# Kernel tuning notes

Measured on AMD Instinct MI355X. Metric: run time of the kernel, lower is better.

Reference implementation:

```python
import jax, jax.numpy as jnp
import numpy as np

N = 8192
F_IN = 1024
F_OUT = 256
ALPHA = 0.2          # LeakyReLU negative slope
ADJ_DENSITY = 0.004  # pre-symmetrization edge probability -> avg degree ~65
NEG_INF = -9.0e15    # matches -9000000000000000.0 in the torch code


def setup_inputs() -> dict:
    key = jax.random.key(0)
    k_h, k_W, k_a, k_adj = jax.random.split(key, 4)
    h = jax.random.normal(k_h, (N, F_IN), dtype=jnp.float32)
    # xavier_uniform with gain=1.414
    lim_W = 1.414 * np.sqrt(6.0 / (F_IN + F_OUT))
    W = jax.random.uniform(k_W, (F_IN, F_OUT), dtype=jnp.float32, minval=-lim_W, maxval=lim_W)
    lim_a = 1.414 * np.sqrt(6.0 / (2 * F_OUT + 1))
    a = jax.random.uniform(k_a, (2 * F_OUT, 1), dtype=jnp.float32, minval=-lim_a, maxval=lim_a)
    # sparse symmetric 0/1 adjacency (float, like the torch code's dense adj)
    u = jax.random.uniform(k_adj, (N, N))
    m = u < ADJ_DENSITY
    adj = (m | m.T).astype(jnp.float32)
    return {"h": h, "adj": adj, "W": W, "a": a}


def reference(h, adj, W, a):
    # --- GAT attention ---
    Wh = h @ W                                   # [N, F_OUT]
    Wh1 = Wh @ a[:F_OUT]                          # [N, 1]
    Wh2 = Wh @ a[F_OUT:]                          # [N, 1]
    e = jax.nn.leaky_relu(Wh1 + Wh2.T, negative_slope=ALPHA)   # [N, N]
    attention = jax.nn.softmax(jnp.where(adj > 0, e, NEG_INF), axis=1)

    # --- per-row variable-k pruning of attention + attention@attention.T ---
    n = adj.shape[0]
    diag = jnp.eye(n, dtype=bool)
    adj_nodiag = jnp.where(diag, 0.0, adj)
    s2 = jnp.count_nonzero(adj_nodiag, axis=1)    # [N] int, variable k per row

    attention2step = attention @ attention.T      # [N, N] dense GEMM
    comb = attention + attention2step
    comb = jnp.where(diag, 0.0, comb)

    # threshold = s2[i]-th largest value of row i (np.partition(row, -k)[-k])
    sorted_desc = -jnp.sort(-comb, axis=1)        # [N, N] descending per row
    idx = jnp.maximum(s2 - 1, 0)[:, None]         # clamp for s2==0 rows
    thr = jnp.take_along_axis(sorted_desc, idx, axis=1)   # [N, 1]
    # keep values >= threshold (torch code zeros values strictly < partition);
    # rows with s2 == 0 are zeroed entirely
    pruned = jnp.where((s2[:, None] > 0) & (comb >= thr), comb, 0.0)
    adj_resize = (pruned > 0).astype(jnp.float32)

    # --- output (eval mode: dropout is identity); concat=True -> ELU ---
    h_prime = attention @ Wh                      # [N, F_OUT]
    return jax.nn.elu(h_prime), adj_resize
```

## Files before the change

### kernel.cpp

```cpp
#include <hip/hip_runtime.h>
#include <cstdint>
#include <cstddef>

#define NN 8192
#define KFIN 1024
#define KFOUT 256
#define MAXD 192
#define LRALPHA 0.2f

typedef float f32x4 __attribute__((ext_vector_type(4)));

__global__ void __launch_bounds__(256) k_build_csr(
    const float* __restrict__ adj, int* __restrict__ nbr,
    int* __restrict__ deg, int* __restrict__ s2v) {
  const int wave = threadIdx.x >> 6;
  const int lane = threadIdx.x & 63;
  const int row = blockIdx.x * 4 + wave;
  const float* arow = adj + (size_t)row * NN;
  int* outp = nbr + (size_t)row * MAXD;
  int count = 0;
  int dflag = 0;
  const unsigned long long below = (1ull << lane) - 1ull;
  for (int c0 = 0; c0 < NN; c0 += 256) {
    const int c = c0 + lane * 4;
    const f32x4 v = __builtin_nontemporal_load(
        reinterpret_cast<const f32x4*>(arow + c));
    const unsigned long long m0 = __ballot(v[0] > 0.0f);
    const unsigned long long m1 = __ballot(v[1] > 0.0f);
    const unsigned long long m2 = __ballot(v[2] > 0.0f);
    const unsigned long long m3 = __ballot(v[3] > 0.0f);
    int pos = count + (int)(__popcll(m0 & below) + __popcll(m1 & below) +
                            __popcll(m2 & below) + __popcll(m3 & below));
    if (v[0] > 0.0f) { if (pos < MAXD) outp[pos] = c + 0; ++pos; if (c + 0 == row) dflag = 1; }
    if (v[1] > 0.0f) { if (pos < MAXD) outp[pos] = c + 1; ++pos; if (c + 1 == row) dflag = 1; }
    if (v[2] > 0.0f) { if (pos < MAXD) outp[pos] = c + 2; ++pos; if (c + 2 == row) dflag = 1; }
    if (v[3] > 0.0f) { if (pos < MAXD) outp[pos] = c + 3; ++pos; if (c + 3 == row) dflag = 1; }
    count += (int)(__popcll(m0) + __popcll(m1) + __popcll(m2) + __popcll(m3));
  }
  const int anyd = __any(dflag) ? 1 : 0;
  if (lane == 0) {
    deg[row] = count < MAXD ? count : MAXD;
    s2v[row] = count - anyd;
  }
}

__global__ void __launch_bounds__(256) k_gemm(
    const float* __restrict__ A, const float* __restrict__ B,
    float* __restrict__ C) {
  __shared__ float As[16][65];
  __shared__ float Bs[16][65];
  const int tid = threadIdx.x;
  const int brow = blockIdx.y * 64;
  const int bcol = blockIdx.x * 64;
  const int tx = tid & 15;
  const int ty = tid >> 4;
  float acc[4][4];
#pragma unroll
  for (int i = 0; i < 4; ++i)
#pragma unroll
    for (int j = 0; j < 4; ++j) acc[i][j] = 0.0f;
  const int ar = tid >> 2;
  const int ac = (tid & 3) << 2;
  const int br = tid >> 4;
  const int bc = (tid & 15) << 2;
  for (int k0 = 0; k0 < KFIN; k0 += 16) {
    const float4 av =
        *reinterpret_cast<const float4*>(A + (size_t)(brow + ar) * KFIN + k0 + ac);
    const float4 bv =
        *reinterpret_cast<const float4*>(B + (size_t)(k0 + br) * KFOUT + bcol + bc);
    As[ac + 0][ar] = av.x;
    As[ac + 1][ar] = av.y;
    As[ac + 2][ar] = av.z;
    As[ac + 3][ar] = av.w;
    Bs[br][bc + 0] = bv.x;
    Bs[br][bc + 1] = bv.y;
    Bs[br][bc + 2] = bv.z;
    Bs[br][bc + 3] = bv.w;
    __syncthreads();
#pragma unroll
    for (int kk = 0; kk < 16; ++kk) {
      const float a0 = As[kk][ty * 4 + 0];
      const float a1 = As[kk][ty * 4 + 1];
      const float a2 = As[kk][ty * 4 + 2];
      const float a3 = As[kk][ty * 4 + 3];
      const float b0 = Bs[kk][tx * 4 + 0];
      const float b1 = Bs[kk][tx * 4 + 1];
      const float b2 = Bs[kk][tx * 4 + 2];
      const float b3 = Bs[kk][tx * 4 + 3];
      acc[0][0] += a0 * b0; acc[0][1] += a0 * b1; acc[0][2] += a0 * b2; acc[0][3] += a0 * b3;
      acc[1][0] += a1 * b0; acc[1][1] += a1 * b1; acc[1][2] += a1 * b2; acc[1][3] += a1 * b3;
      acc[2][0] += a2 * b0; acc[2][1] += a2 * b1; acc[2][2] += a2 * b2; acc[2][3] += a2 * b3;
      acc[3][0] += a3 * b0; acc[3][1] += a3 * b1; acc[3][2] += a3 * b2; acc[3][3] += a3 * b3;
    }
    __syncthreads();
  }
#pragma unroll
  for (int i = 0; i < 4; ++i) {
#pragma unroll
    for (int j = 0; j < 4; ++j) {
      C[(size_t)(brow + ty * 4 + i) * KFOUT + bcol + tx * 4 + j] = acc[i][j];
    }
  }
}

__global__ void __launch_bounds__(256) k_rowdots(
    const float* __restrict__ Wh, const float* __restrict__ a,
    float* __restrict__ Wh1, float* __restrict__ Wh2) {
  __shared__ float sA[256];
  __shared__ float sB[256];
  const int row = blockIdx.x;
  const int t = threadIdx.x;
  const float w = Wh[(size_t)row * KFOUT + t];
  sA[t] = w * a[t];
  sB[t] = w * a[KFOUT + t];
  __syncthreads();
  for (int s = 128; s > 0; s >>= 1) {
    if (t < s) {
      sA[t] += sA[t + s];
      sB[t] += sB[t + s];
    }
    __syncthreads();
  }
  if (t == 0) {
    Wh1[row] = sA[0];
    Wh2[row] = sB[0];
  }
}

__global__ void __launch_bounds__(256) k_stats(
    const int* __restrict__ nbr, const int* __restrict__ deg,
    const float* __restrict__ Wh1, const float* __restrict__ Wh2,
    float* __restrict__ mrow, float* __restrict__ Zrow) {
  const int wave = threadIdx.x >> 6;
  const int lane = threadIdx.x & 63;
  const int row = blockIdx.x * 4 + wave;
  const int d = deg[row];
  const int* cols = nbr + (size_t)row * MAXD;
  const float w1 = Wh1[row];
  float mx = -1e30f;
  for (int t = lane; t < d; t += 64) {
    float e = w1 + Wh2[cols[t]];
    e = e > 0.0f ? e : LRALPHA * e;
    mx = fmaxf(mx, e);
  }
  for (int o = 32; o > 0; o >>= 1) mx = fmaxf(mx, __shfl_xor(mx, o));
  float sum = 0.0f;
  for (int t = lane; t < d; t += 64) {
    float e = w1 + Wh2[cols[t]];
    e = e > 0.0f ? e : LRALPHA * e;
    sum += expf(e - mx);
  }
  for (int o = 32; o > 0; o >>= 1) sum += __shfl_xor(sum, o);
  if (lane == 0) {
    mrow[row] = mx;
    Zrow[row] = (d > 0) ? sum : 1.0f;
  }
}

__global__ void __launch_bounds__(256) k_att(
    const int* __restrict__ nbr, const int* __restrict__ deg,
    const float* __restrict__ Wh1, const float* __restrict__ Wh2,
    const float* __restrict__ mrow, const float* __restrict__ Zrow,
    float* __restrict__ att, int2* __restrict__ edgesT,
    short* __restrict__ qb8) {
  const int wave = threadIdx.x >> 6;
  const int lane = threadIdx.x & 63;
  const int row = blockIdx.x * 4 + wave;
  const int d = deg[row];
  const int* cols = nbr + (size_t)row * MAXD;
  const float w1r = Wh1[row];
  const float w2r = Wh2[row];
  const float mr = mrow[row];
  const float invZr = 1.0f / Zrow[row];
  int b[7] = {0, 0, 0, 0, 0, 0, 0};
  for (int t0 = 0; t0 < d; t0 += 64) {
    const int t = t0 + lane;
    const bool act = t < d;
    const int j = act ? cols[t] : 0x7fffffff;
#pragma unroll
    for (int m = 1; m <= 7; ++m)
      b[m - 1] += (int)__popcll(__ballot(act && j < m * 1024));
    if (act) {
      float e = w1r + Wh2[j];
      e = e > 0.0f ? e : LRALPHA * e;
      att[(size_t)row * MAXD + t] = expf(e - mr) * invZr;
      float e2 = Wh1[j] + w2r;
      e2 = e2 > 0.0f ? e2 : LRALPHA * e2;
      const float v = expf(e2 - mrow[j]) / Zrow[j];
      edgesT[(size_t)row * MAXD + t] = make_int2(j, __float_as_int(v));
    }
  }
  if (lane == 0) {
    short* q = qb8 + (size_t)row * 8;
    q[0] = (short)b[0]; q[1] = (short)b[1]; q[2] = (short)b[2]; q[3] = (short)b[3];
    q[4] = (short)b[4]; q[5] = (short)b[5]; q[6] = (short)b[6]; q[7] = (short)d;
  }
}

__global__ void __launch_bounds__(512) k_twostep(
    const int* __restrict__ nbr, const int* __restrict__ deg,
    const int* __restrict__ s2v, const float* __restrict__ att,
    const int2* __restrict__ edgesT, const short* __restrict__ qb8,
    float* __restrict__ out1) {
  __shared__ float comb[NN];
  __shared__ float wvals[MAXD];
  __shared__ int kcols[MAXD];
  __shared__ int kbase[MAXD];
  __shared__ unsigned short packw[8][MAXD];
  __shared__ unsigned int hist[256];
  __shared__ unsigned int shPrefix;
  __shared__ int shRemaining;
  const int tid = threadIdx.x;
  const int wave = tid >> 6;
  const int lane = tid & 63;
  const int row = blockIdx.x;
  const f32x4 z4 = {0.0f, 0.0f, 0.0f, 0.0f};
  for (int j = tid * 4; j < NN; j += 2048)
    *reinterpret_cast<f32x4*>(&comb[j]) = z4;
  const int d = deg[row];
  const int* cols = nbr + (size_t)row * MAXD;
  const float* arow = att + (size_t)row * MAXD;
  for (int t = tid; t < d; t += 512) {
    const int c = cols[t];
    kcols[t] = c;
    kbase[t] = c * MAXD;
    wvals[t] = arow[t];
    short q[8];
    *reinterpret_cast<int4*>(q) = *reinterpret_cast<const int4*>(&qb8[(size_t)c * 8]);
    int prev = 0;
#pragma unroll
    for (int w = 0; w < 8; ++w) {
      const int qe = (int)q[w];
      packw[w][t] = (unsigned short)(prev | (qe << 8));
      prev = qe;
    }
  }
  __syncthreads();
  {
    const int grp = lane >> 4;
    const int sub = lane & 15;
    const int nsteps = (d + 3) >> 2;
    int2 eA = make_int2(0, 0), eB = make_int2(0, 0);
    float wA = 0.0f, wB = 0.0f;
    bool pA_ = false, pB_ = false;
#define PA_ISSUE(E_, W_, P_, S_)                                       \
    {                                                                   \
      const int t_ = (S_) * 4 + grp;                                    \
      const bool v_ = t_ < d;                                           \
      const unsigned pk_ = v_ ? (unsigned)packw[wave][t_] : 0u;         \
      const int qs_ = (int)(pk_ & 255u);                                \
      const int qe_ = (int)(pk_ >> 8);                                  \
      P_ = v_ && (qs_ + sub) < qe_;                                     \
      W_ = v_ ? wvals[t_] : 0.0f;                                       \
      E_ = make_int2(0, 0);                                             \
      if (P_) E_ = edgesT[(size_t)kbase[t_] + qs_ + sub];               \
    }
    if (nsteps > 0) PA_ISSUE(eA, wA, pA_, 0);
    if (nsteps > 1) PA_ISSUE(eB, wB, pB_, 1);
    for (int s = 0; s < nsteps; ++s) {
      const int2 e = eA; const float w = wA; const bool p = pA_;
      eA = eB; wA = wB; pA_ = pB_;
      if (s + 2 < nsteps) PA_ISSUE(eB, wB, pB_, s + 2);
      if (p) atomicAdd(&comb[e.x], w * __int_as_float(e.y));
    }
#undef PA_ISSUE
  }
  for (int t0 = 0; t0 < d; t0 += 64) {
    const int t = t0 + lane;
    bool big = false;
    if (t < d) {
      const unsigned pk = (unsigned)packw[wave][t];
      big = ((int)(pk >> 8) - (int)(pk & 255u)) > 16;
    }
    unsigned long long m = __ballot(big);
    while (m) {
      const int tt = t0 + (int)__ffsll((long long)m) - 1;
      m &= m - 1;
      const unsigned pk = (unsigned)packw[wave][tt];
      const int qs = (int)(pk & 255u);
      const int qe = (int)(pk >> 8);
      const float w = wvals[tt];
      const int base = kbase[tt];
      for (int off = qs + 16 + lane; off < qe; off += 64) {
        const int2 e = edgesT[(size_t)base + off];
        atomicAdd(&comb[e.x], w * __int_as_float(e.y));
      }
    }
  }
  {
    const short* qr = qb8 + (size_t)row * 8;
    const int qlo = wave ? (int)qr[wave - 1] : 0;
    const int qhi = (int)qr[wave];
    for (int t = qlo + lane; t < qhi; t += 64) comb[kcols[t]] += wvals[t];
  }
  __syncthreads();
  if (tid == 0) comb[row] = 0.0f;
  __syncthreads();
  const int kk = s2v[row];
  const size_t obase = (size_t)row * NN;
  if (kk <= 0) {
    for (int j = tid * 4; j < NN; j += 2048)
      __builtin_nontemporal_store(z4, reinterpret_cast<f32x4*>(&out1[obase + j]));
    return;
  }
  unsigned int prefix = 0u;
  int remaining = kk;
  for (int pass = 0; pass < 4; ++pass) {
    const int shift = 24 - 8 * pass;
    const unsigned int pmask = (pass == 0) ? 0u : (0xFFFFFFFFu << (shift + 8));
    if (tid < 256) hist[tid] = 0u;
    __syncthreads();
    for (int j = tid * 4; j < NN; j += 2048) {
      const f32x4 cv = *reinterpret_cast<const f32x4*>(&comb[j]);
#pragma unroll
      for (int q = 0; q < 4; ++q) {
        const unsigned int u = __float_as_uint(cv[q]);
        if (u != 0u && (u & pmask) == prefix)
          atomicAdd(&hist[(u >> shift) & 255u], 1u);
      }
    }
    __syncthreads();
    if (tid < 64) {
      const int bHi = 255 - 4 * lane;
      const unsigned int c0 = hist[bHi];
      const unsigned int c1 = hist[bHi - 1];
      const unsigned int c2 = hist[bHi - 2];
      const unsigned int c3 = hist[bHi - 3];
      const unsigned int gs = c0 + c1 + c2 + c3;
      unsigned int run2 = gs;
      for (int o = 1; o < 64; o <<= 1) {
        const unsigned int tt = __shfl_up(run2, o);
        if (lane >= o) run2 += tt;
      }
      const unsigned int pre = run2 - gs;
      const unsigned int rem = (unsigned int)remaining;
      if (pre < rem && pre + gs >= rem) {
        unsigned int above;
        int digit;
        if (pre + c0 >= rem) { digit = bHi; above = pre; }
        else if (pre + c0 + c1 >= rem) { digit = bHi - 1; above = pre + c0; }
        else if (pre + c0 + c1 + c2 >= rem) { digit = bHi - 2; above = pre + c0 + c1; }
        else { digit = bHi - 3; above = pre + c0 + c1 + c2; }
        shPrefix = prefix | ((unsigned int)digit << shift);
        shRemaining = remaining - (int)above;
      }
    }
    __syncthreads();
    prefix = shPrefix;
    remaining = shRemaining;
    __syncthreads();
  }
  const float thr = __uint_as_float(prefix);
  for (int j = tid * 4; j < NN; j += 2048) {
    const f32x4 cv = *reinterpret_cast<const f32x4*>(&comb[j]);
    f32x4 ov;
    ov[0] = (cv[0] >= thr && cv[0] > 0.0f) ? 1.0f : 0.0f;
    ov[1] = (cv[1] >= thr && cv[1] > 0.0f) ? 1.0f : 0.0f;
    ov[2] = (cv[2] >= thr && cv[2] > 0.0f) ? 1.0f : 0.0f;
    ov[3] = (cv[3] >= thr && cv[3] > 0.0f) ? 1.0f : 0.0f;
    __builtin_nontemporal_store(ov, reinterpret_cast<f32x4*>(&out1[obase + j]));
  }
}

__global__ void __launch_bounds__(256) k_hprime(
    const int* __restrict__ nbr, const int* __restrict__ deg,
    const float* __restrict__ att, const float* __restrict__ Wh,
    float* __restrict__ out0) {
  __shared__ int scol[MAXD];
  __shared__ float sval[MAXD];
  const int row = blockIdx.x;
  const int c = threadIdx.x;
  const int d = deg[row];
  const int* cols = nbr + (size_t)row * MAXD;
  const float* arow = att + (size_t)row * MAXD;
  for (int t = threadIdx.x; t < d; t += 256) {
    scol[t] = cols[t];
    sval[t] = arow[t];
  }
  __syncthreads();
  float a0 = 0.0f, a1 = 0.0f, a2 = 0.0f, a3 = 0.0f;
  int t = 0;
  for (; t + 4 <= d; t += 4) {
    a0 += sval[t + 0] * Wh[(size_t)scol[t + 0] * KFOUT + c];
    a1 += sval[t + 1] * Wh[(size_t)scol[t + 1] * KFOUT + c];
    a2 += sval[t + 2] * Wh[(size_t)scol[t + 2] * KFOUT + c];
    a3 += sval[t + 3] * Wh[(size_t)scol[t + 3] * KFOUT + c];
  }
  for (; t < d; ++t) a0 += sval[t] * Wh[(size_t)scol[t] * KFOUT + c];
  const float acc = (a0 + a1) + (a2 + a3);
  out0[(size_t)row * KFOUT + c] = acc > 0.0f ? acc : expm1f(acc);
}

extern "C" void kernel_launch(void* const* d_in, const int* in_sizes, int n_in,
                              void* d_out, int out_size, void* d_ws, size_t ws_size,
                              hipStream_t stream) {
  const float* h = (const float*)d_in[0];
  const float* adj = (const float*)d_in[1];
  const float* W = (const float*)d_in[2];
  const float* a = (const float*)d_in[3];

  float* out0 = (float*)d_out;
  float* out1 = out0 + (size_t)NN * KFOUT;

  float* Wh = (float*)d_ws;
  float* Wh1 = Wh + (size_t)NN * KFOUT;
  float* Wh2 = Wh1 + NN;
  float* mrow = Wh2 + NN;
  float* Zrow = mrow + NN;
  float* att = Zrow + NN;
  float* edgesF = att + (size_t)NN * MAXD;
  int2* edgesT = (int2*)edgesF;
  int* nbr = (int*)(edgesF + (size_t)NN * MAXD * 2);
  int* deg = nbr + (size_t)NN * MAXD;
  int* s2v = deg + NN;
  short* qb8 = (short*)(s2v + NN);

  k_build_csr<<<NN / 4, 256, 0, stream>>>(adj, nbr, deg, s2v);
  dim3 ggrid(KFOUT / 64, NN / 64);
  k_gemm<<<ggrid, 256, 0, stream>>>(h, W, Wh);
  k_rowdots<<<NN, 256, 0, stream>>>(Wh, a, Wh1, Wh2);
  k_stats<<<NN / 4, 256, 0, stream>>>(nbr, deg, Wh1, Wh2, mrow, Zrow);
  k_att<<<NN / 4, 256, 0, stream>>>(nbr, deg, Wh1, Wh2, mrow, Zrow, att, edgesT, qb8);
  k_twostep<<<NN, 512, 0, stream>>>(nbr, deg, s2v, att, edgesT, qb8, out1);
  k_hprime<<<NN, 256, 0, stream>>>(nbr, deg, att, Wh, out0);
}
```

Measured before the change: 488.6 us.

## Merge CSR build and GEMM into one launch, deepen twostep prefetch

The CSR-building pass and the h@W GEMM are merged into one kernel with a 1D grid. The first 2048 blocks scan adjacency rows and the remaining 512 compute GEMM tiles, so the bandwidth-bound scan and the compute-bound GEMM can run concurrently and one launch is saved. In the two-step kernel, the per-neighbor qb8 unpacking is spread across all threads (d*8 work items), and the gather-then-atomicAdd software pipeline goes from 2 to 4 stages to hide more load latency. The deeper pipeline costs extra registers, and the unpacking now reads qb8 redundantly.

Result: slower. 544.6 us (+11.5%).

```diff
diff --git a/kernel.cpp b/kernel.cpp
--- a/kernel.cpp
+++ b/kernel.cpp
@@ -10,48 +10,49 @@
 
 typedef float f32x4 __attribute__((ext_vector_type(4)));
 
-__global__ void __launch_bounds__(256) k_build_csr(
+__global__ void __launch_bounds__(256) k_csr_gemm(
     const float* __restrict__ adj, int* __restrict__ nbr,
-    int* __restrict__ deg, int* __restrict__ s2v) {
-  const int wave = threadIdx.x >> 6;
-  const int lane = threadIdx.x & 63;
-  const int row = blockIdx.x * 4 + wave;
-  const float* arow = adj + (size_t)row * NN;
-  int* outp = nbr + (size_t)row * MAXD;
-  int count = 0;
-  int dflag = 0;
-  const unsigned long long below = (1ull << lane) - 1ull;
-  for (int c0 = 0; c0 < NN; c0 += 256) {
-    const int c = c0 + lane * 4;
-    const f32x4 v = __builtin_nontemporal_load(
-        reinterpret_cast<const f32x4*>(arow + c));
-    const unsigned long long m0 = __ballot(v[0] > 0.0f);
-    const unsigned long long m1 = __ballot(v[1] > 0.0f);
-    const unsigned long long m2 = __ballot(v[2] > 0.0f);
-    const unsigned long long m3 = __ballot(v[3] > 0.0f);
-    int pos = count + (int)(__popcll(m0 & below) + __popcll(m1 & below) +
-                            __popcll(m2 & below) + __popcll(m3 & below));
-    if (v[0] > 0.0f) { if (pos < MAXD) outp[pos] = c + 0; ++pos; if (c + 0 == row) dflag = 1; }
-    if (v[1] > 0.0f) { if (pos < MAXD) outp[pos] = c + 1; ++pos; if (c + 1 == row) dflag = 1; }
-    if (v[2] > 0.0f) { if (pos < MAXD) outp[pos] = c + 2; ++pos; if (c + 2 == row) dflag = 1; }
-    if (v[3] > 0.0f) { if (pos < MAXD) outp[pos] = c + 3; ++pos; if (c + 3 == row) dflag = 1; }
-    count += (int)(__popcll(m0) + __popcll(m1) + __popcll(m2) + __popcll(m3));
-  }
-  const int anyd = __any(dflag) ? 1 : 0;
-  if (lane == 0) {
-    deg[row] = count < MAXD ? count : MAXD;
-    s2v[row] = count - anyd;
-  }
-}
-
-__global__ void __launch_bounds__(256) k_gemm(
+    int* __restrict__ deg, int* __restrict__ s2v,
     const float* __restrict__ A, const float* __restrict__ B,
     float* __restrict__ C) {
   __shared__ float As[16][65];
   __shared__ float Bs[16][65];
+  if (blockIdx.x < 2048) {
+    const int wave = threadIdx.x >> 6;
+    const int lane = threadIdx.x & 63;
+    const int row = blockIdx.x * 4 + wave;
+    const float* arow = adj + (size_t)row * NN;
+    int* outp = nbr + (size_t)row * MAXD;
+    int count = 0;
+    int dflag = 0;
+    const unsigned long long below = (1ull << lane) - 1ull;
+    for (int c0 = 0; c0 < NN; c0 += 256) {
+      const int c = c0 + lane * 4;
+      const f32x4 v = __builtin_nontemporal_load(
+          reinterpret_cast<const f32x4*>(arow + c));
+      const unsigned long long m0 = __ballot(v[0] > 0.0f);
+      const unsigned long long m1 = __ballot(v[1] > 0.0f);
+      const unsigned long long m2 = __ballot(v[2] > 0.0f);
+      const unsigned long long m3 = __ballot(v[3] > 0.0f);
+      int pos = count + (int)(__popcll(m0 & below) + __popcll(m1 & below) +
+                              __popcll(m2 & below) + __popcll(m3 & below));
+      if (v[0] > 0.0f) { if (pos < MAXD) outp[pos] = c + 0; ++pos; if (c + 0 == row) dflag = 1; }
+      if (v[1] > 0.0f) { if (pos < MAXD) outp[pos] = c + 1; ++pos; if (c + 1 == row) dflag = 1; }
+      if (v[2] > 0.0f) { if (pos < MAXD) outp[pos] = c + 2; ++pos; if (c + 2 == row) dflag = 1; }
+      if (v[3] > 0.0f) { if (pos < MAXD) outp[pos] = c + 3; ++pos; if (c + 3 == row) dflag = 1; }
+      count += (int)(__popcll(m0) + __popcll(m1) + __popcll(m2) + __popcll(m3));
+    }
+    const int anyd = __any(dflag) ? 1 : 0;
+    if (lane == 0) {
+      deg[row] = count < MAXD ? count : MAXD;
+      s2v[row] = count - anyd;
+    }
+    return;
+  }
+  const int bx = blockIdx.x - 2048;
   const int tid = threadIdx.x;
-  const int brow = blockIdx.y * 64;
-  const int bcol = blockIdx.x * 64;
+  const int brow = (bx >> 2) * 64;
+  const int bcol = (bx & 3) * 64;
   const int tx = tid & 15;
   const int ty = tid >> 4;
   float acc[4][4];
@@ -225,15 +226,14 @@
     kcols[t] = c;
     kbase[t] = c * MAXD;
     wvals[t] = arow[t];
-    short q[8];
-    *reinterpret_cast<int4*>(q) = *reinterpret_cast<const int4*>(&qb8[(size_t)c * 8]);
-    int prev = 0;
-#pragma unroll
-    for (int w = 0; w < 8; ++w) {
-      const int qe = (int)q[w];
-      packw[w][t] = (unsigned short)(prev | (qe << 8));
-      prev = qe;
-    }
+  }
+  for (int tt = tid; tt < d * 8; tt += 512) {
+    const int t = tt >> 3;
+    const int w = tt & 7;
+    const int c = cols[t];
+    const int qe = (int)qb8[(size_t)c * 8 + w];
+    const int qs = w ? (int)qb8[(size_t)c * 8 + w - 1] : 0;
+    packw[w][t] = (unsigned short)(qs | (qe << 8));
   }
   __syncthreads();
   {
@@ -241,8 +241,9 @@
     const int sub = lane & 15;
     const int nsteps = (d + 3) >> 2;
     int2 eA = make_int2(0, 0), eB = make_int2(0, 0);
-    float wA = 0.0f, wB = 0.0f;
-    bool pA_ = false, pB_ = false;
+    int2 eC = make_int2(0, 0), eD = make_int2(0, 0);
+    float wA = 0.0f, wB = 0.0f, wC = 0.0f, wD = 0.0f;
+    bool pA_ = false, pB_ = false, pC_ = false, pD_ = false;
 #define PA_ISSUE(E_, W_, P_, S_)                                       \
     {                                                                   \
       const int t_ = (S_) * 4 + grp;                                    \
@@ -257,10 +258,14 @@
     }
     if (nsteps > 0) PA_ISSUE(eA, wA, pA_, 0);
     if (nsteps > 1) PA_ISSUE(eB, wB, pB_, 1);
+    if (nsteps > 2) PA_ISSUE(eC, wC, pC_, 2);
+    if (nsteps > 3) PA_ISSUE(eD, wD, pD_, 3);
     for (int s = 0; s < nsteps; ++s) {
       const int2 e = eA; const float w = wA; const bool p = pA_;
       eA = eB; wA = wB; pA_ = pB_;
-      if (s + 2 < nsteps) PA_ISSUE(eB, wB, pB_, s + 2);
+      eB = eC; wB = wC; pB_ = pC_;
+      eC = eD; wC = wD; pC_ = pD_;
+      if (s + 4 < nsteps) PA_ISSUE(eD, wD, pD_, s + 4);
       if (p) atomicAdd(&comb[e.x], w * __int_as_float(e.y));
     }
 #undef PA_ISSUE
@@ -415,9 +420,7 @@
   int* s2v = deg + NN;
   short* qb8 = (short*)(s2v + NN);
 
-  k_build_csr<<<NN / 4, 256, 0, stream>>>(adj, nbr, deg, s2v);
-  dim3 ggrid(KFOUT / 64, NN / 64);
-  k_gemm<<<ggrid, 256, 0, stream>>>(h, W, Wh);
+  k_csr_gemm<<<2048 + 512, 256, 0, stream>>>(adj, nbr, deg, s2v, h, W, Wh);
   k_rowdots<<<NN, 256, 0, stream>>>(Wh, a, Wh1, Wh2);
   k_stats<<<NN / 4, 256, 0, stream>>>(nbr, deg, Wh1, Wh2, mrow, Zrow);
   k_att<<<NN / 4, 256, 0, stream>>>(nbr, deg, Wh1, Wh2, mrow, Zrow, att, edgesT, qb8);
```
